# Performance work log

Hardware: AMD Instinct MI355X
Metric: run time of the kernel (lower is better)

## Reference

```python
import jax, jax.numpy as jnp
import numpy as np

TREE_DEPTH = 8
N_INTERNAL = 2 ** TREE_DEPTH - 1   # 255
N_LEAVES = 2 ** TREE_DEPTH         # 256
N_CLASSES = 100
N_TREES = 16
BATCH = 8192
D_FEAT = 1024
TEMPERATURE = 1.0


def setup_inputs() -> dict:
    key = jax.random.key(0)
    k1, k2, k3, k4, k5 = jax.random.split(key, 5)
    x = jax.random.normal(k1, (BATCH, D_FEAT), dtype=jnp.float32)
    # scale weights ~1/sqrt(D) so split logits are O(1) (avoids sigmoid saturation)
    split_weights = jax.random.normal(k2, (N_TREES, N_INTERNAL, D_FEAT), dtype=jnp.float32) / np.sqrt(D_FEAT)
    split_bias = jax.random.normal(k3, (N_TREES, N_INTERNAL), dtype=jnp.float32)
    leaf_logits = jax.random.normal(k4, (N_TREES, N_LEAVES, N_CLASSES), dtype=jnp.float32)
    tree_weights = jax.random.normal(k5, (N_TREES,), dtype=jnp.float32)
    return {"x": x, "split_weights": split_weights, "split_bias": split_bias,
            "leaf_logits": leaf_logits, "tree_weights": tree_weights}


def reference(x, split_weights, split_bias, leaf_logits, tree_weights):
    # All internal-node split logits in one contraction: [T, B, N_INTERNAL]
    logits = jnp.einsum('bd,tnd->tbn', x, split_weights) + split_bias[:, None, :]
    split_prob = jax.nn.sigmoid(logits / TEMPERATURE)  # P(go right) per heap node
    T, B = split_prob.shape[0], split_prob.shape[1]
    # Level-order path products. Heap layout: level d occupies nodes [2^d-1, 2^(d+1)-2].
    # Child j of a node splits into (left=2j, right=2j+1) at next level -> interleave.
    mu = jnp.ones((T, B, 1), dtype=x.dtype)
    for d in range(TREE_DEPTH):
        start = 2 ** d - 1
        p = split_prob[:, :, start:start + 2 ** d]          # [T, B, 2^d]
        mu = jnp.stack([mu * (1.0 - p), mu * p], axis=-1)   # left, right
        mu = mu.reshape(T, B, 2 ** (d + 1))
    # mu: [T, B, N_LEAVES] leaf reach probabilities, ordering matches leaf_idx
    leaf_dist = jax.nn.softmax(leaf_logits, axis=-1)        # [T, L, C]
    per_tree = jnp.einsum('tbl,tlc->tbc', mu, leaf_dist)    # [T, B, C]
    w = jax.nn.softmax(tree_weights, axis=0)[:, None, None]
    return (per_tree * w).sum(axis=0)                       # [B, C]
```

## Files before the change

kernel.cpp:

```cpp
#include <hip/hip_runtime.h>
#include <hip/hip_fp16.h>

typedef _Float16 f16;
typedef _Float16 f16x8 __attribute__((ext_vector_type(8)));
typedef float    f32x4 __attribute__((ext_vector_type(4)));

constexpr int TREES = 16;
constexpr int NNODE = 255;
constexpr int NLEAF = 256;
constexpr int NCLS  = 100;
constexpr int NCPAD = 112;
constexpr int NB    = 8192;
constexpr int DF    = 1024;
constexpr int KTOT  = TREES * NLEAF;

constexpr size_t XH_OFF = 0;
constexpr size_t WH_OFF = XH_OFF + (size_t)NB * DF;
constexpr size_t SD_OFF = WH_OFF + (size_t)TREES * 256 * DF;
constexpr size_t PT_OFF_F = (SD_OFF + (size_t)NCPAD * KTOT) / 2;

__device__ __forceinline__ void gload_lds16(const f16* g, f16* l) {
  __builtin_amdgcn_global_load_lds(
      (const __attribute__((address_space(1))) void*)g,
      (__attribute__((address_space(3))) void*)l, 16, 0, 0);
}

__global__ void cvt_x_k(const float* __restrict__ x, f16* __restrict__ xh) {
  int i = blockIdx.x * 256 + threadIdx.x;
  const float4* s = (const float4*)x + (size_t)i * 2;
  float4 u = s[0], v = s[1];
  f16x8 h = {(f16)u.x, (f16)u.y, (f16)u.z, (f16)u.w,
             (f16)v.x, (f16)v.y, (f16)v.z, (f16)v.w};
  *((f16x8*)xh + i) = h;
}

__global__ void cvt_w_k(const float* __restrict__ w, f16* __restrict__ wh) {
  int i = blockIdx.x * 256 + threadIdx.x;
  int flat = i * 8;
  int t = flat >> 18;
  int r = (flat >> 10) & 255;
  int k = flat & 1023;
  f16x8 h;
  if (r < NNODE) {
    const float4* s = (const float4*)(w + ((size_t)(t * NNODE + r) * DF + k));
    float4 u = s[0], v = s[1];
    h = (f16x8){(f16)u.x, (f16)u.y, (f16)u.z, (f16)u.w,
                (f16)v.x, (f16)v.y, (f16)v.z, (f16)v.w};
  } else {
    h = (f16x8){(f16)0.f, (f16)0.f, (f16)0.f, (f16)0.f,
                (f16)0.f, (f16)0.f, (f16)0.f, (f16)0.f};
  }
  *((f16x8*)wh + i) = h;
}

__global__ void prep_sdist_k(const float* __restrict__ ll,
                             const float* __restrict__ twin,
                             f16* __restrict__ sdt) {
  int id = blockIdx.x * 64 + threadIdx.x;
  int t = id >> 8;
  float wm = -1e30f;
#pragma unroll
  for (int i = 0; i < 16; ++i) wm = fmaxf(wm, twin[i]);
  float wsum = 0.f;
#pragma unroll
  for (int i = 0; i < 16; ++i) wsum += __expf(twin[i] - wm);
  float wt = __expf(twin[t] - wm) / wsum;

  const float* rowp = ll + (size_t)id * NCLS;
  float mx = -1e30f;
  for (int c = 0; c < NCLS; c += 4) {
    float4 v = *(const float4*)(rowp + c);
    mx = fmaxf(fmaxf(fmaxf(mx, v.x), v.y), fmaxf(v.z, v.w));
  }
  float s = 0.f;
  for (int c = 0; c < NCLS; c += 4) {
    float4 v = *(const float4*)(rowp + c);
    s += __expf(v.x - mx) + __expf(v.y - mx) + __expf(v.z - mx) + __expf(v.w - mx);
  }
  float inv = wt / s;
  for (int c = 0; c < NCLS; ++c)
    sdt[(size_t)c * KTOT + id] = (f16)(__expf(rowp[c] - mx) * inv);
  for (int c = NCLS; c < NCPAD; ++c)
    sdt[(size_t)c * KTOT + id] = (f16)0.f;
}

__global__ __launch_bounds__(256, 2) void tree_gemm1(
    const f16* __restrict__ xh, const f16* __restrict__ wh,
    const float* __restrict__ bias, const f16* __restrict__ sdt,
    float* __restrict__ ptree) {
  __shared__ f16 smem[40960];
  f16* A0 = smem;
  f16* B0 = smem + 4096;
  f16* A1 = smem + 20480;
  f16* B1 = smem + 24576;

  const int tid  = threadIdx.x;
  const int lane = tid & 63;
  const int wid  = tid >> 6;
  const int l15  = lane & 15;
  const int lq   = lane >> 4;

  int bid  = blockIdx.x;
  int xcd  = bid & 7;
  int j    = bid >> 3;
  int brow = j & 127;
  int t    = ((j >> 7) << 3) | xcd;

  const f16* xsrc = xh + (size_t)brow * 64 * DF;
  const f16* wsrc = wh + (size_t)t * 256 * DF;

  auto stage = [&](int kt, f16* Ab, f16* Bb) {
    const f16* xk = xsrc + kt * 64;
    const f16* wk = wsrc + kt * 64;
#pragma unroll
    for (int ld = 0; ld < 2; ++ld) {
      int q  = ld * 256 + tid;
      int r  = q >> 3;
      int c0 = (q & 7) ^ (r & 7);
      gload_lds16(xk + (size_t)r * DF + c0 * 8, Ab + q * 8);
    }
#pragma unroll
    for (int ld = 0; ld < 8; ++ld) {
      int q  = ld * 256 + tid;
      int n  = q >> 3;
      int c0 = (q & 7) ^ (n & 7);
      gload_lds16(wk + (size_t)n * DF + c0 * 8, Bb + q * 8);
    }
  };

  f32x4 acc[4][4];
#pragma unroll
  for (int m = 0; m < 4; ++m)
#pragma unroll
    for (int n = 0; n < 4; ++n) acc[m][n] = (f32x4){0.f, 0.f, 0.f, 0.f};

  auto compute = [&](const f16* Ab, const f16* Bb) {
#pragma unroll
    for (int s = 0; s < 2; ++s) {
      f16x8 af[4], bf[4];
#pragma unroll
      for (int m = 0; m < 4; ++m) {
        int r = m * 16 + l15;
        int byteoff = (r * 128 + s * 64 + lq * 16) ^ ((r & 7) << 4);
        af[m] = *(const f16x8*)((const char*)Ab + byteoff);
      }
#pragma unroll
      for (int n = 0; n < 4; ++n) {
        int node = wid * 64 + n * 16 + l15;
        int byteoff = (node * 128 + s * 64 + lq * 16) ^ ((node & 7) << 4);
        bf[n] = *(const f16x8*)((const char*)Bb + byteoff);
      }
#pragma unroll
      for (int m = 0; m < 4; ++m)
#pragma unroll
        for (int n = 0; n < 4; ++n)
          acc[m][n] = __builtin_amdgcn_mfma_f32_16x16x32_f16(af[m], bf[n], acc[m][n], 0, 0, 0);
    }
  };

  stage(0, A0, B0);
  __syncthreads();
  for (int kt = 0; kt < 14; kt += 2) {
    stage(kt + 1, A1, B1);
    compute(A0, B0);
    __syncthreads();
    stage(kt + 2, A0, B0);
    compute(A1, B1);
    __syncthreads();
  }
  stage(15, A1, B1);
  compute(A0, B0);
  __syncthreads();
  compute(A1, B1);

  f16* p_lds = smem;
#pragma unroll
  for (int m = 0; m < 4; ++m) {
#pragma unroll
    for (int n = 0; n < 4; ++n) {
      int col = wid * 64 + n * 16 + l15;
      float bv = (col < NNODE) ? bias[t * NNODE + col] : 0.f;
#pragma unroll
      for (int reg = 0; reg < 4; ++reg) {
        int row = m * 16 + lq * 4 + reg;
        float z = acc[m][n][reg] + bv;
        float p = 1.f / (1.f + __expf(-z));
        p_lds[row * 258 + col] = (f16)p;
      }
    }
  }
  __syncthreads();

  int row   = tid >> 2;
  int chunk = tid & 3;
  const f16* P = p_lds + row * 258;
  float p0 = (float)P[0];
  float p1 = (float)P[1 + (chunk >> 1)];
  float pr = ((chunk >> 1) ? p0 : 1.f - p0) * ((chunk & 1) ? p1 : 1.f - p1);
  float p2 = (float)P[3 + chunk];
  float cur[64];
  {
    float mp = pr * p2;
    cur[1] = mp;
    cur[0] = pr - mp;
  }
#pragma unroll
  for (int d = 3; d <= 7; ++d) {
    int s  = 1 << (d - 2);
    int nb = (1 << d) - 1 + (chunk << (d - 2));
#pragma unroll
    for (int i = s - 1; i >= 0; --i) {
      float p  = (float)P[nb + i];
      float m  = cur[i];
      float mp = m * p;
      cur[2 * i + 1] = mp;
      cur[2 * i]     = m - mp;
    }
  }

  char* mub = (char*)(smem + 18432);
#pragma unroll
  for (int g = 0; g < 8; ++g) {
    f16x8 v;
#pragma unroll
    for (int jj = 0; jj < 8; ++jj) v[jj] = (f16)cur[g * 8 + jj];
    int byteoff = (row * 512 + chunk * 128 + g * 16) ^ ((row & 7) << 4);
    *(f16x8*)(mub + byteoff) = v;
  }
  __syncthreads();

  char* sdb = (char*)smem;
  auto stage_sdt = [&](int c0, int nrows) {
    int nchunks = nrows * 32;
    for (int q = tid; q < nchunks; q += 256) {
      int r = q >> 5;
      int jj = q & 31;
      const f16* src = sdt + (size_t)(c0 + r) * KTOT + t * 256 + ((jj * 8) ^ ((r & 7) << 3));
      gload_lds16(src, smem + q * 8);
    }
  };

  f32x4 acc2[7];
#pragma unroll
  for (int n = 0; n < 7; ++n) acc2[n] = (f32x4){0.f, 0.f, 0.f, 0.f};

  int arow = wid * 16 + l15;
  stage_sdt(0, 64);
  __syncthreads();
#pragma unroll
  for (int n = 0; n < 4; ++n) {
#pragma unroll
    for (int s = 0; s < 8; ++s) {
      int abyte = (arow * 512 + s * 64 + lq * 16) ^ ((arow & 7) << 4);
      f16x8 a = *(const f16x8*)(mub + abyte);
      int br = n * 16 + l15;
      int bbyte = (br * 512 + s * 64 + lq * 16) ^ ((br & 7) << 4);
      f16x8 b = *(const f16x8*)(sdb + bbyte);
      acc2[n] = __builtin_amdgcn_mfma_f32_16x16x32_f16(a, b, acc2[n], 0, 0, 0);
    }
  }
  __syncthreads();
  stage_sdt(64, 48);
  __syncthreads();
#pragma unroll
  for (int n = 4; n < 7; ++n) {
#pragma unroll
    for (int s = 0; s < 8; ++s) {
      int abyte = (arow * 512 + s * 64 + lq * 16) ^ ((arow & 7) << 4);
      f16x8 a = *(const f16x8*)(mub + abyte);
      int br = (n - 4) * 16 + l15;
      int bbyte = (br * 512 + s * 64 + lq * 16) ^ ((br & 7) << 4);
      f16x8 b = *(const f16x8*)(sdb + bbyte);
      acc2[n] = __builtin_amdgcn_mfma_f32_16x16x32_f16(a, b, acc2[n], 0, 0, 0);
    }
  }

  float* pt = ptree + ((size_t)t * NB + brow * 64) * NCLS;
#pragma unroll
  for (int n = 0; n < 7; ++n) {
    int col = n * 16 + l15;
    if (col < NCLS) {
#pragma unroll
      for (int reg = 0; reg < 4; ++reg) {
        int r = wid * 16 + lq * 4 + reg;
        pt[(size_t)r * NCLS + col] = acc2[n][reg];
      }
    }
  }
}

__global__ void reduce_k(const float* __restrict__ pt, float* __restrict__ out) {
  int i = blockIdx.x * 256 + threadIdx.x;
  constexpr size_t STRIDE4 = (size_t)NB * NCLS / 4;
  const float4* p = (const float4*)pt + i;
  float4 s = p[0];
#pragma unroll
  for (int t = 1; t < TREES; ++t) {
    float4 v = p[t * STRIDE4];
    s.x += v.x; s.y += v.y; s.z += v.z; s.w += v.w;
  }
  ((float4*)out)[i] = s;
}

extern "C" void kernel_launch(void* const* d_in, const int* in_sizes, int n_in,
                              void* d_out, int out_size, void* d_ws, size_t ws_size,
                              hipStream_t stream) {
  const float* x  = (const float*)d_in[0];
  const float* sw = (const float*)d_in[1];
  const float* sb = (const float*)d_in[2];
  const float* ll = (const float*)d_in[3];
  const float* tw = (const float*)d_in[4];
  float* out = (float*)d_out;

  f16* ws  = (f16*)d_ws;
  f16* xh  = ws + XH_OFF;
  f16* wh  = ws + WH_OFF;
  f16* sdt = ws + SD_OFF;
  float* ptree = (float*)d_ws + PT_OFF_F;

  cvt_x_k<<<(NB * DF / 8) / 256, 256, 0, stream>>>(x, xh);
  cvt_w_k<<<(TREES * 256 * DF / 8) / 256, 256, 0, stream>>>(sw, wh);
  prep_sdist_k<<<64, 64, 0, stream>>>(ll, tw, sdt);
  tree_gemm1<<<TREES * (NB / 64), 256, 0, stream>>>(xh, wh, sb, sdt, ptree);
  reduce_k<<<(NB * NCLS / 4) / 256, 256, 0, stream>>>(ptree, out);
}
```

Measured before the change: 218.1 us.

## Enlarge GEMM tile to 256 rows with 512-thread blocks and split-stage pipelining

The main tree kernel now uses 512-thread blocks, each computing a 256-row by 256-node tile, so every weight tile staged in LDS is reused across four times as many batch rows. The k-loop double buffer is filled in two halves with explicit vmcnt waits, overlapping loads with MFMA. The sigmoid results are kept in registers and the path-product and leaf GEMM run in two 128-row halves. The two conversion kernels are merged into one, and bias is pre-padded into a workspace buffer so the epilogue can load it as float4. The larger LDS footprint (160KB) and more registers per thread may reduce occupancy.

```diff
diff --git a/kernel.cpp b/kernel.cpp
--- a/kernel.cpp
+++ b/kernel.cpp
@@ -2,22 +2,30 @@
 #include <hip/hip_fp16.h>
 
 typedef _Float16 f16;
+typedef _Float16 f16x4 __attribute__((ext_vector_type(4)));
 typedef _Float16 f16x8 __attribute__((ext_vector_type(8)));
 typedef float    f32x4 __attribute__((ext_vector_type(4)));
 
 constexpr int TREES = 16;
 constexpr int NNODE = 255;
-constexpr int NLEAF = 256;
 constexpr int NCLS  = 100;
 constexpr int NCPAD = 112;
 constexpr int NB    = 8192;
 constexpr int DF    = 1024;
-constexpr int KTOT  = TREES * NLEAF;
+constexpr int KTOT  = TREES * 256;
 
 constexpr size_t XH_OFF = 0;
 constexpr size_t WH_OFF = XH_OFF + (size_t)NB * DF;
 constexpr size_t SD_OFF = WH_OFF + (size_t)TREES * 256 * DF;
-constexpr size_t PT_OFF_F = (SD_OFF + (size_t)NCPAD * KTOT) / 2;
+constexpr size_t BP_OFF = SD_OFF + (size_t)NCPAD * KTOT;
+constexpr size_t PT_OFF_F = (BP_OFF + 8192) / 2;
+
+#define WAIT_VMCNT(n) asm volatile("s_waitcnt vmcnt(" #n ")" ::: "memory")
+__device__ __forceinline__ void BAR() {
+  asm volatile("" ::: "memory");
+  __builtin_amdgcn_s_barrier();
+  asm volatile("" ::: "memory");
+}
 
 __device__ __forceinline__ void gload_lds16(const f16* g, f16* l) {
   __builtin_amdgcn_global_load_lds(
@@ -25,39 +33,46 @@
       (__attribute__((address_space(3))) void*)l, 16, 0, 0);
 }
 
-__global__ void cvt_x_k(const float* __restrict__ x, f16* __restrict__ xh) {
-  int i = blockIdx.x * 256 + threadIdx.x;
-  const float4* s = (const float4*)x + (size_t)i * 2;
-  float4 u = s[0], v = s[1];
-  f16x8 h = {(f16)u.x, (f16)u.y, (f16)u.z, (f16)u.w,
-             (f16)v.x, (f16)v.y, (f16)v.z, (f16)v.w};
-  *((f16x8*)xh + i) = h;
-}
-
-__global__ void cvt_w_k(const float* __restrict__ w, f16* __restrict__ wh) {
-  int i = blockIdx.x * 256 + threadIdx.x;
-  int flat = i * 8;
-  int t = flat >> 18;
-  int r = (flat >> 10) & 255;
-  int k = flat & 1023;
-  f16x8 h;
-  if (r < NNODE) {
-    const float4* s = (const float4*)(w + ((size_t)(t * NNODE + r) * DF + k));
+__global__ void cvt_all_k(const float* __restrict__ x, const float* __restrict__ w,
+                          f16* __restrict__ xh, f16* __restrict__ wh) {
+  int bid = blockIdx.x;
+  if (bid < 4096) {
+    int i = bid * 256 + threadIdx.x;
+    const float4* s = (const float4*)x + (size_t)i * 2;
     float4 u = s[0], v = s[1];
-    h = (f16x8){(f16)u.x, (f16)u.y, (f16)u.z, (f16)u.w,
-                (f16)v.x, (f16)v.y, (f16)v.z, (f16)v.w};
+    f16x8 h = {(f16)u.x, (f16)u.y, (f16)u.z, (f16)u.w,
+               (f16)v.x, (f16)v.y, (f16)v.z, (f16)v.w};
+    *((f16x8*)xh + i) = h;
   } else {
-    h = (f16x8){(f16)0.f, (f16)0.f, (f16)0.f, (f16)0.f,
-                (f16)0.f, (f16)0.f, (f16)0.f, (f16)0.f};
-  }
-  *((f16x8*)wh + i) = h;
+    int i = (bid - 4096) * 256 + threadIdx.x;
+    int flat = i * 8;
+    int t = flat >> 18;
+    int r = (flat >> 10) & 255;
+    int k = flat & 1023;
+    f16x8 h;
+    if (r < NNODE) {
+      const float4* s = (const float4*)(w + ((size_t)(t * NNODE + r) * DF + k));
+      float4 u = s[0], v = s[1];
+      h = (f16x8){(f16)u.x, (f16)u.y, (f16)u.z, (f16)u.w,
+                  (f16)v.x, (f16)v.y, (f16)v.z, (f16)v.w};
+    } else {
+      h = (f16x8){(f16)0.f, (f16)0.f, (f16)0.f, (f16)0.f,
+                  (f16)0.f, (f16)0.f, (f16)0.f, (f16)0.f};
+    }
+    *((f16x8*)wh + i) = h;
+  }
 }
 
 __global__ void prep_sdist_k(const float* __restrict__ ll,
                              const float* __restrict__ twin,
-                             f16* __restrict__ sdt) {
+                             const float* __restrict__ sb,
+                             f16* __restrict__ sdt,
+                             float* __restrict__ bp) {
   int id = blockIdx.x * 64 + threadIdx.x;
   int t = id >> 8;
+  int node = id & 255;
+  bp[id] = (node < NNODE) ? sb[t * NNODE + node] : 0.f;
+
   float wm = -1e30f;
 #pragma unroll
   for (int i = 0; i < 16; ++i) wm = fmaxf(wm, twin[i]);
@@ -84,208 +99,222 @@
     sdt[(size_t)c * KTOT + id] = (f16)0.f;
 }
 
-__global__ __launch_bounds__(256, 2) void tree_gemm1(
+__global__ __launch_bounds__(512, 2) void tree_gemm1(
     const f16* __restrict__ xh, const f16* __restrict__ wh,
-    const float* __restrict__ bias, const f16* __restrict__ sdt,
+    const float* __restrict__ biasp, const f16* __restrict__ sdt,
     float* __restrict__ ptree) {
-  __shared__ f16 smem[40960];
-  f16* A0 = smem;
-  f16* B0 = smem + 4096;
-  f16* A1 = smem + 20480;
-  f16* B1 = smem + 24576;
+  __shared__ f16 smem[81920];
+  char* smb = (char*)smem;
 
   const int tid  = threadIdx.x;
   const int lane = tid & 63;
   const int wid  = tid >> 6;
   const int l15  = lane & 15;
   const int lq   = lane >> 4;
+  const int wrow = (wid >> 2) * 128;
+  const int wcol = (wid & 3) * 64;
 
   int bid  = blockIdx.x;
-  int xcd  = bid & 7;
-  int j    = bid >> 3;
-  int brow = j & 127;
-  int t    = ((j >> 7) << 3) | xcd;
-
-  const f16* xsrc = xh + (size_t)brow * 64 * DF;
+  int t    = (bid & 7) | ((bid >> 8) << 3);
+  int brow = (bid >> 3) & 31;
+
+  const f16* xsrc = xh + (size_t)brow * 256 * DF;
   const f16* wsrc = wh + (size_t)t * 256 * DF;
 
-  auto stage = [&](int kt, f16* Ab, f16* Bb) {
+  auto stage_half = [&](int kt, int c, int half) {
+    f16* Ab = smem + c * 32768;
+    f16* Bb = Ab + 16384;
     const f16* xk = xsrc + kt * 64;
     const f16* wk = wsrc + kt * 64;
 #pragma unroll
-    for (int ld = 0; ld < 2; ++ld) {
-      int q  = ld * 256 + tid;
-      int r  = q >> 3;
-      int c0 = (q & 7) ^ (r & 7);
-      gload_lds16(xk + (size_t)r * DF + c0 * 8, Ab + q * 8);
-    }
-#pragma unroll
-    for (int ld = 0; ld < 8; ++ld) {
-      int q  = ld * 256 + tid;
-      int n  = q >> 3;
-      int c0 = (q & 7) ^ (n & 7);
-      gload_lds16(wk + (size_t)n * DF + c0 * 8, Bb + q * 8);
+    for (int i = half * 2; i < half * 2 + 2; ++i) {
+      int q = i * 512 + tid;
+      int r = q >> 3;
+      int ci = (q & 7) ^ (r & 7);
+      gload_lds16(xk + (size_t)r * DF + ci * 8, Ab + q * 8);
+    }
+#pragma unroll
+    for (int i = half * 2; i < half * 2 + 2; ++i) {
+      int q = i * 512 + tid;
+      int r = q >> 3;
+      int ci = (q & 7) ^ (r & 7);
+      gload_lds16(wk + (size_t)r * DF + ci * 8, Bb + q * 8);
     }
   };
 
-  f32x4 acc[4][4];
-#pragma unroll
-  for (int m = 0; m < 4; ++m)
+  f32x4 acc[8][4];
+#pragma unroll
+  for (int m = 0; m < 8; ++m)
 #pragma unroll
     for (int n = 0; n < 4; ++n) acc[m][n] = (f32x4){0.f, 0.f, 0.f, 0.f};
 
-  auto compute = [&](const f16* Ab, const f16* Bb) {
+  stage_half(0, 0, 0);
+  stage_half(0, 0, 1);
+
+  for (int kt = 0; kt < 16; ++kt) {
+    const int c = kt & 1;
+    if (kt < 15) {
+      stage_half(kt + 1, c ^ 1, 0);
+      WAIT_VMCNT(4);
+    } else {
+      WAIT_VMCNT(0);
+    }
+    BAR();
+
+    const char* Ab = smb + c * 65536;
+    const char* Bb = Ab + 32768;
 #pragma unroll
     for (int s = 0; s < 2; ++s) {
-      f16x8 af[4], bf[4];
-#pragma unroll
-      for (int m = 0; m < 4; ++m) {
-        int r = m * 16 + l15;
-        int byteoff = (r * 128 + s * 64 + lq * 16) ^ ((r & 7) << 4);
-        af[m] = *(const f16x8*)((const char*)Ab + byteoff);
+      f16x8 af[8], bf[4];
+#pragma unroll
+      for (int m = 0; m < 8; ++m) {
+        int r = wrow + m * 16 + l15;
+        af[m] = *(const f16x8*)(Ab + ((r * 128 + s * 64 + lq * 16) ^ ((r & 7) << 4)));
       }
 #pragma unroll
       for (int n = 0; n < 4; ++n) {
-        int node = wid * 64 + n * 16 + l15;
-        int byteoff = (node * 128 + s * 64 + lq * 16) ^ ((node & 7) << 4);
-        bf[n] = *(const f16x8*)((const char*)Bb + byteoff);
-      }
-#pragma unroll
-      for (int m = 0; m < 4; ++m)
+        int node = wcol + n * 16 + l15;
+        bf[n] = *(const f16x8*)(Bb + ((node * 128 + s * 64 + lq * 16) ^ ((node & 7) << 4)));
+      }
+      if (s == 0 && kt < 15) stage_half(kt + 1, c ^ 1, 1);
+#pragma unroll
+      for (int m = 0; m < 8; ++m)
 #pragma unroll
         for (int n = 0; n < 4; ++n)
-          acc[m][n] = __builtin_amdgcn_mfma_f32_16x16x32_f16(af[m], bf[n], acc[m][n], 0, 0, 0);
+          acc[m][n] = __builtin_amdgcn_mfma_f32_16x16x32_f16(bf[n], af[m], acc[m][n], 0, 0, 0);
+    }
+    BAR();
+  }
+
+  f16x4 ph[8][4];
+#pragma unroll
+  for (int m = 0; m < 8; ++m) {
+#pragma unroll
+    for (int n = 0; n < 4; ++n) {
+      int col = wcol + n * 16 + lq * 4;
+      float4 b4 = *(const float4*)(biasp + t * 256 + col);
+#pragma unroll
+      for (int reg = 0; reg < 4; ++reg) {
+        float bv = (reg == 0) ? b4.x : (reg == 1) ? b4.y : (reg == 2) ? b4.z : b4.w;
+        float z = acc[m][n][reg] + bv;
+        ph[m][n][reg] = (f16)__builtin_amdgcn_rcpf(1.f + __expf(-z));
+      }
+    }
+  }
+
+  char* Sb = smb;
+  char* Ub = smb + 32768;
+  char* Pb = smb + 98304;
+
+  auto stage_sdt = [&](int c0, int nrows) {
+    int nch = nrows * 32;
+    for (int q = tid; q < nch; q += 512) {
+      int rr = q >> 5;
+      int jj = q & 31;
+      gload_lds16(sdt + (size_t)(c0 + rr) * KTOT + t * 256 + ((jj * 8) ^ ((rr & 7) << 3)),
+                  smem + q * 8);
     }
   };
 
-  stage(0, A0, B0);
-  __syncthreads();
-  for (int kt = 0; kt < 14; kt += 2) {
-    stage(kt + 1, A1, B1);
-    compute(A0, B0);
-    __syncthreads();
-    stage(kt + 2, A0, B0);
-    compute(A1, B1);
-    __syncthreads();
-  }
-  stage(15, A1, B1);
-  compute(A0, B0);
-  __syncthreads();
-  compute(A1, B1);
-
-  f16* p_lds = smem;
-#pragma unroll
-  for (int m = 0; m < 4; ++m) {
+  for (int h = 0; h < 2; ++h) {
+    if ((wid >> 2) == h) {
+#pragma unroll
+      for (int m = 0; m < 8; ++m) {
+#pragma unroll
+        for (int n = 0; n < 4; ++n) {
+          int r = m * 16 + l15;
+          int colb = (wcol + n * 16 + lq * 4) * 2;
+          *(f16x4*)(Pb + ((r * 512 + colb) ^ ((r & 15) << 3))) = ph[m][n];
+        }
+      }
+    }
+    __syncthreads();
+
+    {
+      int r = tid >> 2;
+      int chunk = tid & 3;
+      auto PR = [&](int node) -> float {
+        return (float)*(const f16*)(Pb + ((r * 512 + node * 2) ^ ((r & 15) << 3)));
+      };
+      float p0 = PR(0);
+      float p1 = PR(1 + (chunk >> 1));
+      float pr = ((chunk >> 1) ? p0 : 1.f - p0) * ((chunk & 1) ? p1 : 1.f - p1);
+      float p2 = PR(3 + chunk);
+      float cur[64];
+      {
+        float mp = pr * p2;
+        cur[1] = mp;
+        cur[0] = pr - mp;
+      }
+#pragma unroll
+      for (int d = 3; d <= 7; ++d) {
+        int sfan = 1 << (d - 2);
+        int nb = (1 << d) - 1 + (chunk << (d - 2));
+#pragma unroll
+        for (int i = sfan - 1; i >= 0; --i) {
+          float p = PR(nb + i);
+          float mv = cur[i];
+          float mp = mv * p;
+          cur[2 * i + 1] = mp;
+          cur[2 * i] = mv - mp;
+        }
+      }
+#pragma unroll
+      for (int g = 0; g < 8; ++g) {
+        f16x8 v;
+#pragma unroll
+        for (int jj = 0; jj < 8; ++jj) v[jj] = (f16)cur[g * 8 + jj];
+        *(f16x8*)(Ub + ((r * 512 + chunk * 128 + g * 16) ^ ((r & 7) << 4))) = v;
+      }
+    }
+    __syncthreads();
+
+    f32x4 acc2[7];
+#pragma unroll
+    for (int n = 0; n < 7; ++n) acc2[n] = (f32x4){0.f, 0.f, 0.f, 0.f};
+    int arow = wid * 16 + l15;
+
+    stage_sdt(0, 64);
+    WAIT_VMCNT(0);
+    __syncthreads();
 #pragma unroll
     for (int n = 0; n < 4; ++n) {
-      int col = wid * 64 + n * 16 + l15;
-      float bv = (col < NNODE) ? bias[t * NNODE + col] : 0.f;
-#pragma unroll
-      for (int reg = 0; reg < 4; ++reg) {
-        int row = m * 16 + lq * 4 + reg;
-        float z = acc[m][n][reg] + bv;
-        float p = 1.f / (1.f + __expf(-z));
-        p_lds[row * 258 + col] = (f16)p;
-      }
-    }
-  }
-  __syncthreads();
-
-  int row   = tid >> 2;
-  int chunk = tid & 3;
-  const f16* P = p_lds + row * 258;
-  float p0 = (float)P[0];
-  float p1 = (float)P[1 + (chunk >> 1)];
-  float pr = ((chunk >> 1) ? p0 : 1.f - p0) * ((chunk & 1) ? p1 : 1.f - p1);
-  float p2 = (float)P[3 + chunk];
-  float cur[64];
-  {
-    float mp = pr * p2;
-    cur[1] = mp;
-    cur[0] = pr - mp;
-  }
-#pragma unroll
-  for (int d = 3; d <= 7; ++d) {
-    int s  = 1 << (d - 2);
-    int nb = (1 << d) - 1 + (chunk << (d - 2));
-#pragma unroll
-    for (int i = s - 1; i >= 0; --i) {
-      float p  = (float)P[nb + i];
-      float m  = cur[i];
-      float mp = m * p;
-      cur[2 * i + 1] = mp;
-      cur[2 * i]     = m - mp;
-    }
-  }
-
-  char* mub = (char*)(smem + 18432);
-#pragma unroll
-  for (int g = 0; g < 8; ++g) {
-    f16x8 v;
-#pragma unroll
-    for (int jj = 0; jj < 8; ++jj) v[jj] = (f16)cur[g * 8 + jj];
-    int byteoff = (row * 512 + chunk * 128 + g * 16) ^ ((row & 7) << 4);
-    *(f16x8*)(mub + byteoff) = v;
-  }
-  __syncthreads();
-
-  char* sdb = (char*)smem;
-  auto stage_sdt = [&](int c0, int nrows) {
-    int nchunks = nrows * 32;
-    for (int q = tid; q < nchunks; q += 256) {
-      int r = q >> 5;
-      int jj = q & 31;
-      const f16* src = sdt + (size_t)(c0 + r) * KTOT + t * 256 + ((jj * 8) ^ ((r & 7) << 3));
-      gload_lds16(src, smem + q * 8);
-    }
-  };
-
-  f32x4 acc2[7];
-#pragma unroll
-  for (int n = 0; n < 7; ++n) acc2[n] = (f32x4){0.f, 0.f, 0.f, 0.f};
-
-  int arow = wid * 16 + l15;
-  stage_sdt(0, 64);
-  __syncthreads();
-#pragma unroll
-  for (int n = 0; n < 4; ++n) {
-#pragma unroll
-    for (int s = 0; s < 8; ++s) {
-      int abyte = (arow * 512 + s * 64 + lq * 16) ^ ((arow & 7) << 4);
-      f16x8 a = *(const f16x8*)(mub + abyte);
-      int br = n * 16 + l15;
-      int bbyte = (br * 512 + s * 64 + lq * 16) ^ ((br & 7) << 4);
-      f16x8 b = *(const f16x8*)(sdb + bbyte);
-      acc2[n] = __builtin_amdgcn_mfma_f32_16x16x32_f16(a, b, acc2[n], 0, 0, 0);
-    }
-  }
-  __syncthreads();
-  stage_sdt(64, 48);
-  __syncthreads();
-#pragma unroll
-  for (int n = 4; n < 7; ++n) {
-#pragma unroll
-    for (int s = 0; s < 8; ++s) {
-      int abyte = (arow * 512 + s * 64 + lq * 16) ^ ((arow & 7) << 4);
-      f16x8 a = *(const f16x8*)(mub + abyte);
-      int br = (n - 4) * 16 + l15;
-      int bbyte = (br * 512 + s * 64 + lq * 16) ^ ((br & 7) << 4);
-      f16x8 b = *(const f16x8*)(sdb + bbyte);
-      acc2[n] = __builtin_amdgcn_mfma_f32_16x16x32_f16(a, b, acc2[n], 0, 0, 0);
-    }
-  }
-
-  float* pt = ptree + ((size_t)t * NB + brow * 64) * NCLS;
-#pragma unroll
-  for (int n = 0; n < 7; ++n) {
-    int col = n * 16 + l15;
-    if (col < NCLS) {
-#pragma unroll
-      for (int reg = 0; reg < 4; ++reg) {
-        int r = wid * 16 + lq * 4 + reg;
-        pt[(size_t)r * NCLS + col] = acc2[n][reg];
-      }
-    }
+#pragma unroll
+      for (int s = 0; s < 8; ++s) {
+        f16x8 a = *(const f16x8*)(Ub + ((arow * 512 + s * 64 + lq * 16) ^ ((arow & 7) << 4)));
+        int br = n * 16 + l15;
+        f16x8 b = *(const f16x8*)(Sb + ((br * 512 + s * 64 + lq * 16) ^ ((br & 7) << 4)));
+        acc2[n] = __builtin_amdgcn_mfma_f32_16x16x32_f16(a, b, acc2[n], 0, 0, 0);
+      }
+    }
+    __syncthreads();
+    stage_sdt(64, 48);
+    WAIT_VMCNT(0);
+    __syncthreads();
+#pragma unroll
+    for (int n = 4; n < 7; ++n) {
+#pragma unroll
+      for (int s = 0; s < 8; ++s) {
+        f16x8 a = *(const f16x8*)(Ub + ((arow * 512 + s * 64 + lq * 16) ^ ((arow & 7) << 4)));
+        int br = (n - 4) * 16 + l15;
+        f16x8 b = *(const f16x8*)(Sb + ((br * 512 + s * 64 + lq * 16) ^ ((br & 7) << 4)));
+        acc2[n] = __builtin_amdgcn_mfma_f32_16x16x32_f16(a, b, acc2[n], 0, 0, 0);
+      }
+    }
+
+    float* pt = ptree + ((size_t)t * NB + brow * 256 + h * 128) * NCLS;
+#pragma unroll
+    for (int n = 0; n < 7; ++n) {
+      int col = n * 16 + l15;
+      if (col < NCLS) {
+#pragma unroll
+        for (int reg = 0; reg < 4; ++reg) {
+          int r = wid * 16 + lq * 4 + reg;
+          pt[(size_t)r * NCLS + col] = acc2[n][reg];
+        }
+      }
+    }
+    if (h == 0) __syncthreads();
   }
 }
 
@@ -316,11 +345,11 @@
   f16* xh  = ws + XH_OFF;
   f16* wh  = ws + WH_OFF;
   f16* sdt = ws + SD_OFF;
+  float* biasp = (float*)(ws + BP_OFF);
   float* ptree = (float*)d_ws + PT_OFF_F;
 
-  cvt_x_k<<<(NB * DF / 8) / 256, 256, 0, stream>>>(x, xh);
-  cvt_w_k<<<(TREES * 256 * DF / 8) / 256, 256, 0, stream>>>(sw, wh);
-  prep_sdist_k<<<64, 64, 0, stream>>>(ll, tw, sdt);
-  tree_gemm1<<<TREES * (NB / 64), 256, 0, stream>>>(xh, wh, sb, sdt, ptree);
+  cvt_all_k<<<6144, 256, 0, stream>>>(x, sw, xh, wh);
+  prep_sdist_k<<<64, 64, 0, stream>>>(ll, tw, sb, sdt, biasp);
+  tree_gemm1<<<512, 512, 0, stream>>>(xh, wh, biasp, sdt, ptree);
   reduce_k<<<(NB * NCLS / 4) / 256, 256, 0, stream>>>(ptree, out);
 }
```

Measured after the change: 227.7 us. +4.4%, slower.
